# Performance work log

Hardware: AMD Instinct MI355X
Metric: run time of the kernel (lower is better)

## Reference

```python
import jax, jax.numpy as jnp
import numpy as np

HIDDEN = 150
EMBED = 300
OUT = 5
VOCAB = 100000
DEPTH = 13                      # complete binary tree
N = 2 ** DEPTH - 1              # 8191 nodes
L = 2 ** (DEPTH - 1)            # 4096 leaves
SCALE = 0.01


def _build_tree():
    # heap layout: node i internal iff i < N - L; children 2i+1, 2i+2
    words = np.full(N, -1, dtype=np.int64)
    rng = np.random.RandomState(0)
    words[N - L:] = rng.randint(0, VOCAB, size=L)
    lchs = np.zeros(N, dtype=np.int64)
    rchs = np.zeros(N, dtype=np.int64)
    internal = np.arange(N - L)
    lchs[internal] = 2 * internal + 1
    rchs[internal] = 2 * internal + 2
    scores = rng.randint(0, OUT, size=N).astype(np.int64)
    return scores, words, lchs, rchs


def setup_inputs() -> dict:
    key = jax.random.key(0)
    ks = jax.random.split(key, 24)
    p = lambda i, shp: jax.random.normal(ks[i], shp, dtype=jnp.float32) * SCALE
    scores, words, lchs, rchs = _build_tree()
    return {
        "Wi": p(0, (HIDDEN, EMBED)), "bi": p(1, (HIDDEN,)),
        "Wo": p(2, (HIDDEN, EMBED)), "bo": p(3, (HIDDEN,)),
        "Wu": p(4, (HIDDEN, EMBED)), "bu": p(5, (HIDDEN,)),
        "U0i": p(6, (HIDDEN, HIDDEN)), "U1i": p(7, (HIDDEN, HIDDEN)), "bbi": p(8, (HIDDEN,)),
        "U00f": p(9, (HIDDEN, HIDDEN)), "U01f": p(10, (HIDDEN, HIDDEN)),
        "U10f": p(11, (HIDDEN, HIDDEN)), "U11f": p(12, (HIDDEN, HIDDEN)), "bbf": p(13, (HIDDEN,)),
        "U0o": p(14, (HIDDEN, HIDDEN)), "U1o": p(15, (HIDDEN, HIDDEN)), "bbo": p(16, (HIDDEN,)),
        "U0u": p(17, (HIDDEN, HIDDEN)), "U1u": p(18, (HIDDEN, HIDDEN)), "bbu": p(19, (HIDDEN,)),
        "Why": p(20, (OUT, HIDDEN)), "by": p(21, (OUT,)),
        "word_embedding": jax.random.normal(ks[22], (VOCAB, EMBED), dtype=jnp.float32),
        "scores": jnp.asarray(scores), "words": jnp.asarray(words),
        "lchs": jnp.asarray(lchs), "rchs": jnp.asarray(rchs),
    }


def _tree_loss(Wi, bi, Wo, bo, Wu, bu, U0i, U1i, bbi, U00f, U01f, U10f, U11f,
               bbf, U0o, U1o, bbo, U0u, U1u, bbu, Why, by, word_embedding,
               scores, words, lchs, rchs):
    n = scores.shape[0]
    depth = int(np.log2(n + 1))
    leaf_start = 2 ** (depth - 1) - 1

    H_all = jnp.zeros((n, HIDDEN), dtype=Wi.dtype)
    C_all = jnp.zeros((n, HIDDEN), dtype=Wi.dtype)

    # leaf level (batched): cell = sigmoid(Wi e + bi) * tanh(Wu e + bu)
    emb = word_embedding[words[leaf_start:]]              # [L, 300]
    ig = jax.nn.sigmoid(emb @ Wi.T + bi)
    og = jax.nn.sigmoid(emb @ Wo.T + bo)
    uv = jnp.tanh(emb @ Wu.T + bu)
    c = ig * uv
    h = og * jnp.tanh(c)
    H_all = H_all.at[leaf_start:].set(h)
    C_all = C_all.at[leaf_start:].set(c)

    # internal levels, children-before-parents (level-wise batched Tree-LSTM)
    for d in range(depth - 2, -1, -1):
        s, e = 2 ** d - 1, 2 ** (d + 1) - 1
        li, ri = lchs[s:e], rchs[s:e]
        lh, rh = H_all[li], H_all[ri]
        lc, rc = C_all[li], C_all[ri]
        ig = jax.nn.sigmoid(lh @ U0i.T + rh @ U1i.T + bbi)
        fl = jax.nn.sigmoid(lh @ U00f.T + rh @ U01f.T + bbf)
        fr = jax.nn.sigmoid(lh @ U10f.T + rh @ U11f.T + bbf)
        og = jax.nn.sigmoid(lh @ U0o.T + rh @ U1o.T + bbo)
        uv = jnp.tanh(lh @ U0u.T + rh @ U1u.T + bbu)
        c = ig * uv + fl * lc + fr * rc
        h = og * jnp.tanh(c)
        H_all = H_all.at[s:e].set(h)
        C_all = C_all.at[s:e].set(c)

    # per-node NLL loss, summed over all nodes
    logits = H_all @ Why.T + by                            # [N, 5]
    logp = jax.nn.log_softmax(logits, axis=1)
    return -jnp.sum(logp[jnp.arange(n), scores])


def reference(Wi, bi, Wo, bo, Wu, bu, U0i, U1i, bbi, U00f, U01f, U10f, U11f,
              bbf, U0o, U1o, bbo, U0u, U1u, bbu, Why, by, word_embedding,
              scores, words, lchs, rchs):
    return _tree_loss(Wi, bi, Wo, bo, Wu, bu, U0i, U1i, bbi, U00f, U01f,
                      U10f, U11f, bbf, U0o, U1o, bbo, U0u, U1u, bbu, Why, by,
                      word_embedding, scores, words, lchs, rchs)
```

## Files before the change

### kernel.cpp

```cpp
#include <hip/hip_runtime.h>
#include <math.h>

#define HID 150
#define EMB 300
#define NOUT 5
#define NNODES 8191
#define NLEAF 4096
#define LEAF_START 4095
#define HSTR 152
#define UCOLS 768
#define WCOLS 452

constexpr int LOSS_BLOCKS = 64;

__device__ __forceinline__ float sigmoidf_(float x) { return 1.0f / (1.0f + __expf(-x)); }

__global__ __launch_bounds__(256) void prep_kernel(
    const float* __restrict__ Wi, const float* __restrict__ Wo, const float* __restrict__ Wu,
    const float* __restrict__ U0i, const float* __restrict__ U1i,
    const float* __restrict__ U00f, const float* __restrict__ U01f,
    const float* __restrict__ U10f, const float* __restrict__ U11f,
    const float* __restrict__ U0o, const float* __restrict__ U1o,
    const float* __restrict__ U0u, const float* __restrict__ U1u,
    float* __restrict__ Wt2, float* __restrict__ Ut3, float* __restrict__ Ut4)
{
    int idx = blockIdx.x * 256 + threadIdx.x;
    if (idx < EMB * WCOLS) {
        int e = idx / WCOLS, j = idx - e * WCOLS;
        float v = 0.f;
        if (j < 450) {
            const float* W; int h;
            if (j < 150)      { W = Wi; h = j; }
            else if (j < 300) { W = Wo; h = j - 150; }
            else              { W = Wu; h = j - 300; }
            v = W[h * EMB + e];
        }
        Wt2[idx] = v;
    }
    if (idx < EMB * UCOLS) {
        int e = idx / UCOLS, j = idx - e * UCOLS;
        const float* U0[5] = {U0i, U00f, U10f, U0o, U0u};
        const float* U1[5] = {U1i, U01f, U11f, U1o, U1u};
        {
            int hc = j >> 8, cw = j & 255;
            float v = 0.f;
            if (cw < 250) {
                int g = cw / 50, hp = cw - g * 50, h = hc * 50 + hp;
                v = (e < 150) ? U0[g][h * HID + e] : U1[g][h * HID + (e - 150)];
            }
            Ut3[idx] = v;
        }
        {
            int hc = j >> 7, cw = j & 127;
            float v = 0.f;
            if (cw < 125) {
                int g = cw / 25, hp = cw - g * 25, h = hc * 25 + hp;
                v = (e < 150) ? U0[g][h * HID + e] : U1[g][h * HID + (e - 150)];
            }
            Ut4[idx] = v;
        }
    }
}

__global__ __launch_bounds__(512) void leaf_v4(
    const float* __restrict__ Wt2,
    const float* __restrict__ bi, const float* __restrict__ bo, const float* __restrict__ bu,
    const float* __restrict__ emb, const int* __restrict__ words,
    float* __restrict__ H, float* __restrict__ C)
{
    constexpr int NB = 16;
    __shared__ __align__(16) float Xs[EMB * NB];
    __shared__ __align__(16) float Gs[2][NB][WCOLS];
    __shared__ int wq[NB];
    const int tid = threadIdx.x;
    const int leaf0 = LEAF_START + blockIdx.x * NB;

    if (tid < NB) wq[tid] = words[leaf0 + tid];
    __syncthreads();

    for (int p = tid; p < NB * EMB; p += 512) {
        int m = p / EMB, e = p - m * EMB;
        Xs[e * NB + m] = emb[(long)wq[m] * EMB + e];
    }
    __syncthreads();

    {
        const int kq = tid >> 8;
        const int c = tid & 255;
        if (c < 226) {
            float acc[NB][2];
#pragma unroll
            for (int m = 0; m < NB; ++m) { acc[m][0] = 0.f; acc[m][1] = 0.f; }

            const int kbase = kq * 150;
            const float* wp = Wt2 + (long)kbase * WCOLS + 2 * c;
            const float* xp = Xs + kbase * NB;
#pragma unroll 2
            for (int k = 0; k < 150; ++k) {
                float2 w = *(const float2*)(wp + (long)k * WCOLS);
                float4 a0 = *(const float4*)(xp + k * NB);
                float4 a1 = *(const float4*)(xp + k * NB + 4);
                float4 a2 = *(const float4*)(xp + k * NB + 8);
                float4 a3 = *(const float4*)(xp + k * NB + 12);
                float x[NB] = {a0.x, a0.y, a0.z, a0.w, a1.x, a1.y, a1.z, a1.w,
                               a2.x, a2.y, a2.z, a2.w, a3.x, a3.y, a3.z, a3.w};
#pragma unroll
                for (int m = 0; m < NB; ++m) {
                    acc[m][0] = fmaf(x[m], w.x, acc[m][0]);
                    acc[m][1] = fmaf(x[m], w.y, acc[m][1]);
                }
            }
#pragma unroll
            for (int m = 0; m < NB; ++m)
                *(float2*)&Gs[kq][m][2 * c] = make_float2(acc[m][0], acc[m][1]);
        }
    }
    __syncthreads();

    for (int p = tid; p < NB * HID; p += 512) {
        int m = p / HID, h = p - m * HID;
        float gi = Gs[0][m][h]       + Gs[1][m][h];
        float go = Gs[0][m][150 + h] + Gs[1][m][150 + h];
        float gu = Gs[0][m][300 + h] + Gs[1][m][300 + h];
        float ig = sigmoidf_(gi + bi[h]);
        float og = sigmoidf_(go + bo[h]);
        float uv = tanhf(gu + bu[h]);
        float cc = ig * uv;
        float hh = og * tanhf(cc);
        long node = leaf0 + m;
        H[node * HSTR + h] = hh;
        C[node * HSTR + h] = cc;
    }
}

__global__ __launch_bounds__(512) void level_h3w(
    const float* __restrict__ Ut3,
    const float* __restrict__ bbi, const float* __restrict__ bbf,
    const float* __restrict__ bbo, const float* __restrict__ bbu,
    const int* __restrict__ lchs, const int* __restrict__ rchs,
    float* __restrict__ H, float* __restrict__ C, int s)
{
    constexpr int NB = 16;
    __shared__ __align__(16) float Xs[EMB * NB];
    __shared__ __align__(16) float Gs[2][NB][256];
    __shared__ int lidx[NB], ridx[NB];
    const int tid = threadIdx.x;
    const int grp = blockIdx.x / 3, hc = blockIdx.x % 3;
    const int node0 = s + grp * NB;

    if (tid < NB) {
        lidx[tid] = lchs[node0 + tid];
        ridx[tid] = rchs[node0 + tid];
    }
    __syncthreads();

    for (int p = tid; p < NB * EMB; p += 512) {
        int m = p / EMB, e = p - m * EMB;
        Xs[e * NB + m] = (e < HID) ? H[(long)lidx[m] * HSTR + e]
                                   : H[(long)ridx[m] * HSTR + (e - HID)];
    }
    __syncthreads();

    {
        const int kq = tid >> 8, c = tid & 255;
        float acc[NB];
#pragma unroll
        for (int m = 0; m < NB; ++m) acc[m] = 0.f;

        const float* wp = Ut3 + (long)(kq * 150) * UCOLS + hc * 256 + c;
        const float* xp = Xs + (kq * 150) * NB;
#pragma unroll 2
        for (int k = 0; k < 150; ++k) {
            float w = wp[(long)k * UCOLS];
            float4 a0 = *(const float4*)(xp + k * NB);
            float4 a1 = *(const float4*)(xp + k * NB + 4);
            float4 a2 = *(const float4*)(xp + k * NB + 8);
            float4 a3 = *(const float4*)(xp + k * NB + 12);
            float x[NB] = {a0.x, a0.y, a0.z, a0.w, a1.x, a1.y, a1.z, a1.w,
                           a2.x, a2.y, a2.z, a2.w, a3.x, a3.y, a3.z, a3.w};
#pragma unroll
            for (int m = 0; m < NB; ++m) acc[m] = fmaf(x[m], w, acc[m]);
        }
#pragma unroll
        for (int m = 0; m < NB; ++m) Gs[kq][m][c] = acc[m];
    }
    __syncthreads();

    for (int p = tid; p < NB * 50; p += 512) {
        int m = p / 50, hp = p - m * 50, h = hc * 50 + hp;
        float gi  = Gs[0][m][hp]       + Gs[1][m][hp];
        float gf0 = Gs[0][m][50 + hp]  + Gs[1][m][50 + hp];
        float gf1 = Gs[0][m][100 + hp] + Gs[1][m][100 + hp];
        float go  = Gs[0][m][150 + hp] + Gs[1][m][150 + hp];
        float gu  = Gs[0][m][200 + hp] + Gs[1][m][200 + hp];
        float ig = sigmoidf_(gi + bbi[h]);
        float fl = sigmoidf_(gf0 + bbf[h]);
        float fr = sigmoidf_(gf1 + bbf[h]);
        float og = sigmoidf_(go + bbo[h]);
        float uv = tanhf(gu + bbu[h]);
        float lc = C[(long)lidx[m] * HSTR + h];
        float rc = C[(long)ridx[m] * HSTR + h];
        float cc = ig * uv + fl * lc + fr * rc;
        float hh = og * tanhf(cc);
        long node = node0 + m;
        H[node * HSTR + h] = hh;
        C[node * HSTR + h] = cc;
    }
}

template<int NB>
__global__ __launch_bounds__(512) void level_h3(
    const float* __restrict__ Ut3,
    const float* __restrict__ bbi, const float* __restrict__ bbf,
    const float* __restrict__ bbo, const float* __restrict__ bbu,
    const int* __restrict__ lchs, const int* __restrict__ rchs,
    float* __restrict__ H, float* __restrict__ C, int s)
{
    __shared__ __align__(16) float Xs[EMB * NB];
    __shared__ __align__(16) float Gs[4][NB][256];
    __shared__ int lidx[NB], ridx[NB];
    const int tid = threadIdx.x;
    const int grp = blockIdx.x / 3, hc = blockIdx.x % 3;
    const int node0 = s + grp * NB;

    if (tid < NB) {
        lidx[tid] = lchs[node0 + tid];
        ridx[tid] = rchs[node0 + tid];
    }
    __syncthreads();

    for (int p = tid; p < NB * EMB; p += 512) {
        int m = p / EMB, e = p - m * EMB;
        Xs[e * NB + m] = (e < HID) ? H[(long)lidx[m] * HSTR + e]
                                   : H[(long)ridx[m] * HSTR + (e - HID)];
    }
    __syncthreads();

    {
        const int kq = tid >> 7, c2 = tid & 127;
        float acc[NB][2];
#pragma unroll
        for (int m = 0; m < NB; ++m) { acc[m][0] = 0.f; acc[m][1] = 0.f; }

        const float* wp = Ut3 + (long)(kq * 75) * UCOLS + hc * 256 + 2 * c2;
        const float* xp = Xs + (kq * 75) * NB;
#pragma unroll 5
        for (int k = 0; k < 75; ++k) {
            float2 w = *(const float2*)(wp + (long)k * UCOLS);
            float x[NB];
            if constexpr (NB == 8) {
                float4 a = *(const float4*)(xp + k * 8);
                float4 b = *(const float4*)(xp + k * 8 + 4);
                x[0]=a.x; x[1]=a.y; x[2]=a.z; x[3]=a.w;
                x[4]=b.x; x[5]=b.y; x[6]=b.z; x[7]=b.w;
            } else if constexpr (NB == 4) {
                float4 a = *(const float4*)(xp + k * 4);
                x[0]=a.x; x[1]=a.y; x[2]=a.z; x[3]=a.w;
            } else if constexpr (NB == 2) {
                float2 a = *(const float2*)(xp + k * 2);
                x[0]=a.x; x[1]=a.y;
            } else {
                x[0] = xp[k];
            }
#pragma unroll
            for (int m = 0; m < NB; ++m) {
                acc[m][0] = fmaf(x[m], w.x, acc[m][0]);
                acc[m][1] = fmaf(x[m], w.y, acc[m][1]);
            }
        }
#pragma unroll
        for (int m = 0; m < NB; ++m)
            *(float2*)&Gs[kq][m][2 * c2] = make_float2(acc[m][0], acc[m][1]);
    }
    __syncthreads();

    for (int p = tid; p < NB * 50; p += 512) {
        int m = p / 50, hp = p - m * 50, h = hc * 50 + hp;
        float gi  = Gs[0][m][hp]       + Gs[1][m][hp]       + Gs[2][m][hp]       + Gs[3][m][hp];
        float gf0 = Gs[0][m][50 + hp]  + Gs[1][m][50 + hp]  + Gs[2][m][50 + hp]  + Gs[3][m][50 + hp];
        float gf1 = Gs[0][m][100 + hp] + Gs[1][m][100 + hp] + Gs[2][m][100 + hp] + Gs[3][m][100 + hp];
        float go  = Gs[0][m][150 + hp] + Gs[1][m][150 + hp] + Gs[2][m][150 + hp] + Gs[3][m][150 + hp];
        float gu  = Gs[0][m][200 + hp] + Gs[1][m][200 + hp] + Gs[2][m][200 + hp] + Gs[3][m][200 + hp];
        float ig = sigmoidf_(gi + bbi[h]);
        float fl = sigmoidf_(gf0 + bbf[h]);
        float fr = sigmoidf_(gf1 + bbf[h]);
        float og = sigmoidf_(go + bbo[h]);
        float uv = tanhf(gu + bbu[h]);
        float lc = C[(long)lidx[m] * HSTR + h];
        float rc = C[(long)ridx[m] * HSTR + h];
        float cc = ig * uv + fl * lc + fr * rc;
        float hh = og * tanhf(cc);
        long node = node0 + m;
        H[node * HSTR + h] = hh;
        C[node * HSTR + h] = cc;
    }
}

__global__ __launch_bounds__(512) void level_h6(
    const float* __restrict__ Ut4,
    const float* __restrict__ bbi, const float* __restrict__ bbf,
    const float* __restrict__ bbo, const float* __restrict__ bbu,
    const int* __restrict__ lchs, const int* __restrict__ rchs,
    float* __restrict__ H, float* __restrict__ C, int s)
{
    __shared__ __align__(16) float Xs[EMB];
    __shared__ __align__(16) float Gs[4][128];
    __shared__ int lr[2];
    const int tid = threadIdx.x;
    const int grp = blockIdx.x / 6, hc = blockIdx.x % 6;
    const int node = s + grp;

    if (tid < 2) lr[tid] = tid ? rchs[node] : lchs[node];
    __syncthreads();
    if (tid < EMB)
        Xs[tid] = (tid < HID) ? H[(long)lr[0] * HSTR + tid] : H[(long)lr[1] * HSTR + (tid - HID)];
    __syncthreads();

    {
        const int kq = tid >> 7, c = tid & 127;
        float acc = 0.f;
        const float* wp = Ut4 + (long)(kq * 75) * UCOLS + hc * 128 + c;
        const float* xp = Xs + kq * 75;
#pragma unroll 15
        for (int k = 0; k < 75; ++k)
            acc = fmaf(xp[k], wp[(long)k * UCOLS], acc);
        Gs[kq][c] = acc;
    }
    __syncthreads();

    if (tid < 25) {
        int hp = tid, h = hc * 25 + hp;
        float gi  = Gs[0][hp]       + Gs[1][hp]       + Gs[2][hp]       + Gs[3][hp];
        float gf0 = Gs[0][25 + hp]  + Gs[1][25 + hp]  + Gs[2][25 + hp]  + Gs[3][25 + hp];
        float gf1 = Gs[0][50 + hp]  + Gs[1][50 + hp]  + Gs[2][50 + hp]  + Gs[3][50 + hp];
        float go  = Gs[0][75 + hp]  + Gs[1][75 + hp]  + Gs[2][75 + hp]  + Gs[3][75 + hp];
        float gu  = Gs[0][100 + hp] + Gs[1][100 + hp] + Gs[2][100 + hp] + Gs[3][100 + hp];
        float ig = sigmoidf_(gi + bbi[h]);
        float fl = sigmoidf_(gf0 + bbf[h]);
        float fr = sigmoidf_(gf1 + bbf[h]);
        float og = sigmoidf_(go + bbo[h]);
        float uv = tanhf(gu + bbu[h]);
        float lc = C[(long)lr[0] * HSTR + h];
        float rc = C[(long)lr[1] * HSTR + h];
        float cc = ig * uv + fl * lc + fr * rc;
        float hh = og * tanhf(cc);
        H[(long)node * HSTR + h] = hh;
        C[(long)node * HSTR + h] = cc;
    }
}

__global__ __launch_bounds__(256) void loss_kernel(
    const float* __restrict__ H, const float* __restrict__ Why,
    const float* __restrict__ by, const int* __restrict__ scores,
    float* __restrict__ partials)
{
    __shared__ __align__(16) float Wys[NOUT][HSTR];
    __shared__ float bys[NOUT];
    __shared__ float red[256];
    int tid = threadIdx.x;
    for (int i = tid; i < NOUT * HID; i += 256) {
        int g = i / HID, k = i - g * HID;
        Wys[g][k] = Why[g * HID + k];
    }
    if (tid < NOUT) bys[tid] = by[tid];
    __syncthreads();

    float local = 0.f;
    for (int n = blockIdx.x * 256 + tid; n < NNODES; n += gridDim.x * 256) {
        const float* hr = H + (long)n * HSTR;
        float l0 = bys[0], l1 = bys[1], l2 = bys[2], l3 = bys[3], l4 = bys[4];
        for (int k = 0; k < 148; k += 4) {
            float4 hv = *(const float4*)(hr + k);
            float4 w0 = *(const float4*)&Wys[0][k];
            float4 w1 = *(const float4*)&Wys[1][k];
            float4 w2 = *(const float4*)&Wys[2][k];
            float4 w3 = *(const float4*)&Wys[3][k];
            float4 w4 = *(const float4*)&Wys[4][k];
            l0 += hv.x*w0.x + hv.y*w0.y + hv.z*w0.z + hv.w*w0.w;
            l1 += hv.x*w1.x + hv.y*w1.y + hv.z*w1.z + hv.w*w1.w;
            l2 += hv.x*w2.x + hv.y*w2.y + hv.z*w2.z + hv.w*w2.w;
            l3 += hv.x*w3.x + hv.y*w3.y + hv.z*w3.z + hv.w*w3.w;
            l4 += hv.x*w4.x + hv.y*w4.y + hv.z*w4.z + hv.w*w4.w;
        }
        for (int k = 148; k < HID; ++k) {
            float hv = hr[k];
            l0 += hv * Wys[0][k]; l1 += hv * Wys[1][k]; l2 += hv * Wys[2][k];
            l3 += hv * Wys[3][k]; l4 += hv * Wys[4][k];
        }
        float mx = fmaxf(fmaxf(fmaxf(l0, l1), fmaxf(l2, l3)), l4);
        float se = __expf(l0 - mx) + __expf(l1 - mx) + __expf(l2 - mx) +
                   __expf(l3 - mx) + __expf(l4 - mx);
        float lse = mx + __logf(se);
        int sc = scores[n];
        float lsc = (sc == 0) ? l0 : (sc == 1) ? l1 : (sc == 2) ? l2 : (sc == 3) ? l3 : l4;
        local += lse - lsc;
    }
    red[tid] = local;
    __syncthreads();
    for (int st = 128; st > 0; st >>= 1) {
        if (tid < st) red[tid] += red[tid + st];
        __syncthreads();
    }
    if (tid == 0) partials[blockIdx.x] = red[0];
}

__global__ void loss_final(const float* __restrict__ partials, float* __restrict__ out, int nparts)
{
    if (threadIdx.x == 0 && blockIdx.x == 0) {
        float s = 0.f;
        for (int i = 0; i < nparts; ++i) s += partials[i];
        out[0] = s;
    }
}

extern "C" void kernel_launch(void* const* d_in, const int* in_sizes, int n_in,
                              void* d_out, int out_size, void* d_ws, size_t ws_size,
                              hipStream_t stream)
{
    const float* Wi   = (const float*)d_in[0];
    const float* bi   = (const float*)d_in[1];
    const float* Wo   = (const float*)d_in[2];
    const float* bo   = (const float*)d_in[3];
    const float* Wu   = (const float*)d_in[4];
    const float* bu   = (const float*)d_in[5];
    const float* U0i  = (const float*)d_in[6];
    const float* U1i  = (const float*)d_in[7];
    const float* bbi  = (const float*)d_in[8];
    const float* U00f = (const float*)d_in[9];
    const float* U01f = (const float*)d_in[10];
    const float* U10f = (const float*)d_in[11];
    const float* U11f = (const float*)d_in[12];
    const float* bbf  = (const float*)d_in[13];
    const float* U0o  = (const float*)d_in[14];
    const float* U1o  = (const float*)d_in[15];
    const float* bbo  = (const float*)d_in[16];
    const float* U0u  = (const float*)d_in[17];
    const float* U1u  = (const float*)d_in[18];
    const float* bbu  = (const float*)d_in[19];
    const float* Why  = (const float*)d_in[20];
    const float* by   = (const float*)d_in[21];
    const float* emb  = (const float*)d_in[22];
    const int* scores = (const int*)d_in[23];
    const int* words  = (const int*)d_in[24];
    const int* lchs   = (const int*)d_in[25];
    const int* rchs   = (const int*)d_in[26];

    float* ws = (float*)d_ws;
    float* Wt2 = ws;
    float* Ut3 = Wt2 + EMB * WCOLS;
    float* Ut4 = Ut3 + EMB * UCOLS;
    float* H   = Ut4 + EMB * UCOLS;
    float* C   = H + (long)NNODES * HSTR;
    float* partials = C + (long)NNODES * HSTR;
    float* out = (float*)d_out;

    hipLaunchKernelGGL(prep_kernel, dim3(900), dim3(256), 0, stream,
                       Wi, Wo, Wu, U0i, U1i, U00f, U01f, U10f, U11f,
                       U0o, U1o, U0u, U1u, Wt2, Ut3, Ut4);

    hipLaunchKernelGGL(leaf_v4, dim3(NLEAF / 16), dim3(512), 0, stream,
                       Wt2, bi, bo, bu, emb, words, H, C);

    for (int d = 11; d >= 0; --d) {
        int s = (1 << d) - 1, count = 1 << d;
        if (d >= 10) {
            hipLaunchKernelGGL(level_h3w, dim3((count / 16) * 3), dim3(512), 0, stream,
                               Ut3, bbi, bbf, bbo, bbu, lchs, rchs, H, C, s);
        } else if (d == 9) {
            hipLaunchKernelGGL(HIP_KERNEL_NAME(level_h3<8>), dim3((count / 8) * 3), dim3(512), 0, stream,
                               Ut3, bbi, bbf, bbo, bbu, lchs, rchs, H, C, s);
        } else if (d == 8) {
            hipLaunchKernelGGL(HIP_KERNEL_NAME(level_h3<4>), dim3((count / 4) * 3), dim3(512), 0, stream,
                               Ut3, bbi, bbf, bbo, bbu, lchs, rchs, H, C, s);
        } else if (d == 7) {
            hipLaunchKernelGGL(HIP_KERNEL_NAME(level_h3<2>), dim3((count / 2) * 3), dim3(512), 0, stream,
                               Ut3, bbi, bbf, bbo, bbu, lchs, rchs, H, C, s);
        } else {
            hipLaunchKernelGGL(level_h6, dim3(count * 6), dim3(512), 0, stream,
                               Ut4, bbi, bbf, bbo, bbu, lchs, rchs, H, C, s);
        }
    }

    hipLaunchKernelGGL(loss_kernel, dim3(LOSS_BLOCKS), dim3(256), 0, stream,
                       H, Why, by, scores, partials);
    hipLaunchKernelGGL(loss_final, dim3(1), dim3(64), 0, stream,
                       partials, out, LOSS_BLOCKS);
}
```

Measured before the change: 370.8 us.

## Fuse small tree levels and loss into one persistent kernel with grid barriers

```diff
diff --git a/kernel.cpp b/kernel.cpp
--- a/kernel.cpp
+++ b/kernel.cpp
@@ -11,9 +11,31 @@
 #define UCOLS 768
 #define WCOLS 452
 
-constexpr int LOSS_BLOCKS = 64;
+#define TB 384
+#define TT 256
+
+constexpr int LOSS_BLOCKS = TB;
 
 __device__ __forceinline__ float sigmoidf_(float x) { return 1.0f / (1.0f + __expf(-x)); }
+
+__device__ __forceinline__ void grid_barrier(int* bar, int nblk) {
+    __threadfence();
+    __syncthreads();
+    if (threadIdx.x == 0) {
+        int* cnt = bar;
+        int* gen = bar + 1;
+        int g = __hip_atomic_load(gen, __ATOMIC_RELAXED, __HIP_MEMORY_SCOPE_AGENT);
+        if (__hip_atomic_fetch_add(cnt, 1, __ATOMIC_ACQ_REL, __HIP_MEMORY_SCOPE_AGENT) == nblk - 1) {
+            __hip_atomic_store(cnt, 0, __ATOMIC_RELAXED, __HIP_MEMORY_SCOPE_AGENT);
+            __hip_atomic_fetch_add(gen, 1, __ATOMIC_RELEASE, __HIP_MEMORY_SCOPE_AGENT);
+        } else {
+            while (__hip_atomic_load(gen, __ATOMIC_ACQUIRE, __HIP_MEMORY_SCOPE_AGENT) == g)
+                __builtin_amdgcn_s_sleep(1);
+        }
+    }
+    __syncthreads();
+    __threadfence();
+}
 
 __global__ __launch_bounds__(256) void prep_kernel(
     const float* __restrict__ Wi, const float* __restrict__ Wo, const float* __restrict__ Wu,
@@ -22,9 +44,11 @@
     const float* __restrict__ U10f, const float* __restrict__ U11f,
     const float* __restrict__ U0o, const float* __restrict__ U1o,
     const float* __restrict__ U0u, const float* __restrict__ U1u,
-    float* __restrict__ Wt2, float* __restrict__ Ut3, float* __restrict__ Ut4)
+    float* __restrict__ Wt2, float* __restrict__ Ut3, float* __restrict__ Ut4,
+    int* __restrict__ bar)
 {
     int idx = blockIdx.x * 256 + threadIdx.x;
+    if (idx < 2) bar[idx] = 0;
     if (idx < EMB * WCOLS) {
         int e = idx / WCOLS, j = idx - e * WCOLS;
         float v = 0.f;
@@ -296,120 +320,137 @@
     }
 }
 
-__global__ __launch_bounds__(512) void level_h6(
+__global__ __launch_bounds__(TT) void tail_coop(
     const float* __restrict__ Ut4,
     const float* __restrict__ bbi, const float* __restrict__ bbf,
     const float* __restrict__ bbo, const float* __restrict__ bbu,
     const int* __restrict__ lchs, const int* __restrict__ rchs,
-    float* __restrict__ H, float* __restrict__ C, int s)
+    float* __restrict__ H, float* __restrict__ C,
+    const float* __restrict__ Why, const float* __restrict__ by,
+    const int* __restrict__ scores,
+    float* __restrict__ partials, float* __restrict__ out, int* __restrict__ bar)
 {
     __shared__ __align__(16) float Xs[EMB];
-    __shared__ __align__(16) float Gs[4][128];
+    __shared__ __align__(16) float Gs[2][128];
     __shared__ int lr[2];
-    const int tid = threadIdx.x;
-    const int grp = blockIdx.x / 6, hc = blockIdx.x % 6;
-    const int node = s + grp;
-
-    if (tid < 2) lr[tid] = tid ? rchs[node] : lchs[node];
-    __syncthreads();
-    if (tid < EMB)
-        Xs[tid] = (tid < HID) ? H[(long)lr[0] * HSTR + tid] : H[(long)lr[1] * HSTR + (tid - HID)];
-    __syncthreads();
-
-    {
-        const int kq = tid >> 7, c = tid & 127;
-        float acc = 0.f;
-        const float* wp = Ut4 + (long)(kq * 75) * UCOLS + hc * 128 + c;
-        const float* xp = Xs + kq * 75;
-#pragma unroll 15
-        for (int k = 0; k < 75; ++k)
-            acc = fmaf(xp[k], wp[(long)k * UCOLS], acc);
-        Gs[kq][c] = acc;
-    }
-    __syncthreads();
-
-    if (tid < 25) {
-        int hp = tid, h = hc * 25 + hp;
-        float gi  = Gs[0][hp]       + Gs[1][hp]       + Gs[2][hp]       + Gs[3][hp];
-        float gf0 = Gs[0][25 + hp]  + Gs[1][25 + hp]  + Gs[2][25 + hp]  + Gs[3][25 + hp];
-        float gf1 = Gs[0][50 + hp]  + Gs[1][50 + hp]  + Gs[2][50 + hp]  + Gs[3][50 + hp];
-        float go  = Gs[0][75 + hp]  + Gs[1][75 + hp]  + Gs[2][75 + hp]  + Gs[3][75 + hp];
-        float gu  = Gs[0][100 + hp] + Gs[1][100 + hp] + Gs[2][100 + hp] + Gs[3][100 + hp];
-        float ig = sigmoidf_(gi + bbi[h]);
-        float fl = sigmoidf_(gf0 + bbf[h]);
-        float fr = sigmoidf_(gf1 + bbf[h]);
-        float og = sigmoidf_(go + bbo[h]);
-        float uv = tanhf(gu + bbu[h]);
-        float lc = C[(long)lr[0] * HSTR + h];
-        float rc = C[(long)lr[1] * HSTR + h];
-        float cc = ig * uv + fl * lc + fr * rc;
-        float hh = og * tanhf(cc);
-        H[(long)node * HSTR + h] = hh;
-        C[(long)node * HSTR + h] = cc;
-    }
-}
-
-__global__ __launch_bounds__(256) void loss_kernel(
-    const float* __restrict__ H, const float* __restrict__ Why,
-    const float* __restrict__ by, const int* __restrict__ scores,
-    float* __restrict__ partials)
-{
     __shared__ __align__(16) float Wys[NOUT][HSTR];
     __shared__ float bys[NOUT];
-    __shared__ float red[256];
-    int tid = threadIdx.x;
-    for (int i = tid; i < NOUT * HID; i += 256) {
-        int g = i / HID, k = i - g * HID;
-        Wys[g][k] = Why[g * HID + k];
-    }
-    if (tid < NOUT) bys[tid] = by[tid];
-    __syncthreads();
+    __shared__ float red[TT];
+    const int tid = threadIdx.x;
+    const int bid = blockIdx.x;
+
+    for (int d = 6; d >= 0; --d) {
+        const int cnt = 1 << d, s = cnt - 1;
+        const int units = cnt * 6;
+        if (bid < units) {
+            const int grp = bid / 6, hc = bid - grp * 6;
+            const int node = s + grp;
+
+            if (tid < 2) lr[tid] = tid ? rchs[node] : lchs[node];
+            __syncthreads();
+            for (int e = tid; e < EMB; e += TT)
+                Xs[e] = (e < HID) ? H[(long)lr[0] * HSTR + e]
+                                  : H[(long)lr[1] * HSTR + (e - HID)];
+            __syncthreads();
+
+            {
+                const int kq = tid >> 7, c = tid & 127;
+                float a0 = 0.f, a1 = 0.f;
+                const float* wp = Ut4 + (long)(kq * 150) * UCOLS + hc * 128 + c;
+                const float* xp = Xs + kq * 150;
+#pragma unroll 10
+                for (int k = 0; k < 150; k += 2) {
+                    a0 = fmaf(xp[k],     wp[(long)k * UCOLS], a0);
+                    a1 = fmaf(xp[k + 1], wp[(long)(k + 1) * UCOLS], a1);
+                }
+                Gs[kq][c] = a0 + a1;
+            }
+            __syncthreads();
+
+            if (tid < 25) {
+                int hp = tid, h = hc * 25 + hp;
+                float gi  = Gs[0][hp]       + Gs[1][hp];
+                float gf0 = Gs[0][25 + hp]  + Gs[1][25 + hp];
+                float gf1 = Gs[0][50 + hp]  + Gs[1][50 + hp];
+                float go  = Gs[0][75 + hp]  + Gs[1][75 + hp];
+                float gu  = Gs[0][100 + hp] + Gs[1][100 + hp];
+                float ig = sigmoidf_(gi + bbi[h]);
+                float fl = sigmoidf_(gf0 + bbf[h]);
+                float fr = sigmoidf_(gf1 + bbf[h]);
+                float og = sigmoidf_(go + bbo[h]);
+                float uv = tanhf(gu + bbu[h]);
+                float lc = C[(long)lr[0] * HSTR + h];
+                float rc = C[(long)lr[1] * HSTR + h];
+                float cc = ig * uv + fl * lc + fr * rc;
+                float hh = og * tanhf(cc);
+                H[(long)node * HSTR + h] = hh;
+                C[(long)node * HSTR + h] = cc;
+            }
+            __syncthreads();
+        }
+        grid_barrier(bar, TB);
+    }
 
     float local = 0.f;
-    for (int n = blockIdx.x * 256 + tid; n < NNODES; n += gridDim.x * 256) {
-        const float* hr = H + (long)n * HSTR;
-        float l0 = bys[0], l1 = bys[1], l2 = bys[2], l3 = bys[3], l4 = bys[4];
-        for (int k = 0; k < 148; k += 4) {
-            float4 hv = *(const float4*)(hr + k);
-            float4 w0 = *(const float4*)&Wys[0][k];
-            float4 w1 = *(const float4*)&Wys[1][k];
-            float4 w2 = *(const float4*)&Wys[2][k];
-            float4 w3 = *(const float4*)&Wys[3][k];
-            float4 w4 = *(const float4*)&Wys[4][k];
-            l0 += hv.x*w0.x + hv.y*w0.y + hv.z*w0.z + hv.w*w0.w;
-            l1 += hv.x*w1.x + hv.y*w1.y + hv.z*w1.z + hv.w*w1.w;
-            l2 += hv.x*w2.x + hv.y*w2.y + hv.z*w2.z + hv.w*w2.w;
-            l3 += hv.x*w3.x + hv.y*w3.y + hv.z*w3.z + hv.w*w3.w;
-            l4 += hv.x*w4.x + hv.y*w4.y + hv.z*w4.z + hv.w*w4.w;
-        }
-        for (int k = 148; k < HID; ++k) {
-            float hv = hr[k];
-            l0 += hv * Wys[0][k]; l1 += hv * Wys[1][k]; l2 += hv * Wys[2][k];
-            l3 += hv * Wys[3][k]; l4 += hv * Wys[4][k];
-        }
-        float mx = fmaxf(fmaxf(fmaxf(l0, l1), fmaxf(l2, l3)), l4);
-        float se = __expf(l0 - mx) + __expf(l1 - mx) + __expf(l2 - mx) +
-                   __expf(l3 - mx) + __expf(l4 - mx);
-        float lse = mx + __logf(se);
-        int sc = scores[n];
-        float lsc = (sc == 0) ? l0 : (sc == 1) ? l1 : (sc == 2) ? l2 : (sc == 3) ? l3 : l4;
-        local += lse - lsc;
+    if (bid * TT < NNODES) {
+        for (int i = tid; i < NOUT * HID; i += TT) {
+            int g = i / HID, k = i - g * HID;
+            Wys[g][k] = Why[g * HID + k];
+        }
+        if (tid < NOUT) bys[tid] = by[tid];
+        __syncthreads();
+
+        int n = bid * TT + tid;
+        if (n < NNODES) {
+            const float* hr = H + (long)n * HSTR;
+            float l0 = bys[0], l1 = bys[1], l2 = bys[2], l3 = bys[3], l4 = bys[4];
+            for (int k = 0; k < 148; k += 4) {
+                float4 hv = *(const float4*)(hr + k);
+                float4 w0 = *(const float4*)&Wys[0][k];
+                float4 w1 = *(const float4*)&Wys[1][k];
+                float4 w2 = *(const float4*)&Wys[2][k];
+                float4 w3 = *(const float4*)&Wys[3][k];
+                float4 w4 = *(const float4*)&Wys[4][k];
+                l0 += hv.x*w0.x + hv.y*w0.y + hv.z*w0.z + hv.w*w0.w;
+                l1 += hv.x*w1.x + hv.y*w1.y + hv.z*w1.z + hv.w*w1.w;
+                l2 += hv.x*w2.x + hv.y*w2.y + hv.z*w2.z + hv.w*w2.w;
+                l3 += hv.x*w3.x + hv.y*w3.y + hv.z*w3.z + hv.w*w3.w;
+                l4 += hv.x*w4.x + hv.y*w4.y + hv.z*w4.z + hv.w*w4.w;
+            }
+            for (int k = 148; k < HID; ++k) {
+                float hv = hr[k];
+                l0 += hv * Wys[0][k]; l1 += hv * Wys[1][k]; l2 += hv * Wys[2][k];
+                l3 += hv * Wys[3][k]; l4 += hv * Wys[4][k];
+            }
+            float mx = fmaxf(fmaxf(fmaxf(l0, l1), fmaxf(l2, l3)), l4);
+            float se = __expf(l0 - mx) + __expf(l1 - mx) + __expf(l2 - mx) +
+                       __expf(l3 - mx) + __expf(l4 - mx);
+            float lse = mx + __logf(se);
+            int sc = scores[n];
+            float lsc = (sc == 0) ? l0 : (sc == 1) ? l1 : (sc == 2) ? l2 : (sc == 3) ? l3 : l4;
+            local = lse - lsc;
+        }
     }
     red[tid] = local;
     __syncthreads();
-    for (int st = 128; st > 0; st >>= 1) {
+    for (int st = TT / 2; st > 0; st >>= 1) {
         if (tid < st) red[tid] += red[tid + st];
         __syncthreads();
     }
-    if (tid == 0) partials[blockIdx.x] = red[0];
-}
-
-__global__ void loss_final(const float* __restrict__ partials, float* __restrict__ out, int nparts)
-{
-    if (threadIdx.x == 0 && blockIdx.x == 0) {
-        float s = 0.f;
-        for (int i = 0; i < nparts; ++i) s += partials[i];
-        out[0] = s;
+    if (tid == 0) partials[bid] = red[0];
+
+    grid_barrier(bar, TB);
+
+    if (bid == 0) {
+        float v = (tid < TB) ? partials[tid] : 0.f;
+        v += (tid + TT < TB) ? partials[tid + TT] : 0.f;
+        red[tid] = v;
+        __syncthreads();
+        for (int st = TT / 2; st > 0; st >>= 1) {
+            if (tid < st) red[tid] += red[tid + st];
+            __syncthreads();
+        }
+        if (tid == 0) out[0] = red[0];
     }
 }
 
@@ -452,16 +493,17 @@
     float* H   = Ut4 + EMB * UCOLS;
     float* C   = H + (long)NNODES * HSTR;
     float* partials = C + (long)NNODES * HSTR;
+    int*   bar = (int*)(partials + TB);
     float* out = (float*)d_out;
 
     hipLaunchKernelGGL(prep_kernel, dim3(900), dim3(256), 0, stream,
                        Wi, Wo, Wu, U0i, U1i, U00f, U01f, U10f, U11f,
-                       U0o, U1o, U0u, U1u, Wt2, Ut3, Ut4);
+                       U0o, U1o, U0u, U1u, Wt2, Ut3, Ut4, bar);
 
     hipLaunchKernelGGL(leaf_v4, dim3(NLEAF / 16), dim3(512), 0, stream,
                        Wt2, bi, bo, bu, emb, words, H, C);
 
-    for (int d = 11; d >= 0; --d) {
+    for (int d = 11; d >= 7; --d) {
         int s = (1 << d) - 1, count = 1 << d;
         if (d >= 10) {
             hipLaunchKernelGGL(level_h3w, dim3((count / 16) * 3), dim3(512), 0, stream,
@@ -472,17 +514,13 @@
         } else if (d == 8) {
             hipLaunchKernelGGL(HIP_KERNEL_NAME(level_h3<4>), dim3((count / 4) * 3), dim3(512), 0, stream,
                                Ut3, bbi, bbf, bbo, bbu, lchs, rchs, H, C, s);
-        } else if (d == 7) {
+        } else {
             hipLaunchKernelGGL(HIP_KERNEL_NAME(level_h3<2>), dim3((count / 2) * 3), dim3(512), 0, stream,
                                Ut3, bbi, bbf, bbo, bbu, lchs, rchs, H, C, s);
-        } else {
-            hipLaunchKernelGGL(level_h6, dim3(count * 6), dim3(512), 0, stream,
-                               Ut4, bbi, bbf, bbo, bbu, lchs, rchs, H, C, s);
-        }
-    }
-
-    hipLaunchKernelGGL(loss_kernel, dim3(LOSS_BLOCKS), dim3(256), 0, stream,
-                       H, Why, by, scores, partials);
-    hipLaunchKernelGGL(loss_final, dim3(1), dim3(64), 0, stream,
-                       partials, out, LOSS_BLOCKS);
-}
+        }
+    }
+
+    hipLaunchKernelGGL(tail_coop, dim3(TB), dim3(TT), 0, stream,
+                       Ut4, bbi, bbf, bbo, bbu, lchs, rchs, H, C,
+                       Why, by, scores, partials, out, bar);
+}
```

New measurement: 1.414 ms. 281% more time.
